# Kernel tuning notes

Measured on AMD Instinct MI355X. Metric: run time of the kernel, lower is better.

Reference implementation:

```python
import jax, jax.numpy as jnp
import numpy as np

ACTIVE_TASK = 0
K = 4  # top-k experts

def setup_inputs() -> dict:
    key = jax.random.key(0)
    k1, k2, k3, k4 = jax.random.split(key, 4)
    B, L, H, E, T = 16, 8192, 768, 16, 8
    x = jax.random.normal(k1, (B, L, H), jnp.float32)
    task_full = jax.random.normal(k2, (T, H), jnp.float32)
    gate_w = jax.random.normal(k3, (H, E), jnp.float32) * 0.02   # f_gate Linear weight (transposed)
    gate_b = jnp.zeros((E,), jnp.float32)                         # f_gate Linear bias
    expert_w = jax.random.normal(k4, (E, H, H), jnp.float32) * 0.02  # ParallelExperts weight [E, in, out]
    return {"x": x, "task_full": task_full, "gate_w": gate_w, "gate_b": gate_b, "expert_w": expert_w}

def reference(x, task_full, gate_w, gate_b, expert_w):
    T = task_full.shape[0]
    E = gate_w.shape[1]
    # f_gate = SiLU -> Linear
    logits = jax.nn.silu(task_full) @ gate_w + gate_b            # [T, E]
    probs = jax.nn.softmax(logits, axis=1)                       # [T, E]
    top_k_gates, top_k_indices = jax.lax.top_k(probs, K)         # [T, K]
    # probs_full_quantized: one-hot mask of selected experts per task
    probs_full_quantized = jnp.zeros((T, E), jnp.float32).at[
        jnp.arange(T)[:, None], top_k_indices].set(1.0)
    active_probs = probs[ACTIVE_TASK]                            # [E]
    gates = top_k_gates[ACTIVE_TASK]                             # [K]
    idx = top_k_indices[ACTIVE_TASK]                             # [K] int
    # compute_gating on a single task row: batch_index = arange(K)//K == 0 for all
    # slots, so every selected expert consumes a copy of x[0] (length rows each),
    # and index_add accumulates all K weighted expert outputs into out[0].
    h = jnp.einsum('ld,kdo->klo', x[0], expert_w[idx])           # grouped expert GEMM [K, L, H]
    out0 = jnp.einsum('k,klo->lo', gates, h)                     # gate-weighted combine [L, H]
    out = jnp.zeros_like(x).at[0].add(out0)                      # scatter-add at batch_index (all 0)
    return 1.0 + out, active_probs, probs_full_quantized
```

## Files before the change

### kernel.cpp

```cpp
#include <hip/hip_runtime.h>
#include <hip/hip_bf16.h>

typedef __attribute__((ext_vector_type(8))) short short8;
typedef __attribute__((ext_vector_type(4))) float f32x4;

#define H_DIM 768
#define E_EXP 16
#define T_TASK 8
#define KSEL 4
#define L_SEQ 8192
#define B_BATCH 16
#define EW_STRIDE (768*768)

#define WCT_BLOCKS 576
#define FILLA_BLOCKS 1472
#define GEMM_BLOCKS 384
#define FILLB_BLOCKS 1472
#define AS_LD 40

__device__ __forceinline__ void gating_block(
    const float* __restrict__ task_full,
    const float* __restrict__ gate_w,
    const float* __restrict__ gate_b,
    float* silu_s, float (*logits)[E_EXP],
    float* g_sh, int* i_sh,
    float* __restrict__ out_tail, bool write_tail) {
  const int tid = threadIdx.x;
  for (int i = tid; i < T_TASK * H_DIM; i += 256) {
    float v = task_full[i];
    silu_s[i] = v / (1.f + expf(-v));
  }
  __syncthreads();
  if (tid < T_TASK * E_EXP) {
    const int t = tid >> 4, e = tid & 15;
    float a0 = 0.f, a1 = 0.f, a2 = 0.f, a3 = 0.f;
    const float* sl = &silu_s[t * H_DIM];
    for (int h = 0; h < H_DIM; h += 4) {
      a0 += sl[h]     * gate_w[(h)     * E_EXP + e];
      a1 += sl[h + 1] * gate_w[(h + 1) * E_EXP + e];
      a2 += sl[h + 2] * gate_w[(h + 2) * E_EXP + e];
      a3 += sl[h + 3] * gate_w[(h + 3) * E_EXP + e];
    }
    logits[t][e] = (a0 + a1) + (a2 + a3) + gate_b[e];
  }
  __syncthreads();
  if (tid < T_TASK) {
    const int t = tid;
    float p[E_EXP];
    float m = -1e30f;
    for (int e = 0; e < E_EXP; ++e) m = fmaxf(m, logits[t][e]);
    float s = 0.f;
    for (int e = 0; e < E_EXP; ++e) { p[e] = expf(logits[t][e] - m); s += p[e]; }
    const float inv = 1.f / s;
    for (int e = 0; e < E_EXP; ++e) p[e] *= inv;
    bool used[E_EXP];
    for (int e = 0; e < E_EXP; ++e) used[e] = false;
    float g[KSEL]; int sel[KSEL];
    for (int k = 0; k < KSEL; ++k) {
      float bv = -1.f; int bi = 0;
      for (int e = 0; e < E_EXP; ++e)
        if (!used[e] && p[e] > bv) { bv = p[e]; bi = e; }
      used[bi] = true; sel[k] = bi; g[k] = bv;
    }
    if (write_tail) {
      for (int e = 0; e < E_EXP; ++e)
        out_tail[E_EXP + t * E_EXP + e] = used[e] ? 1.f : 0.f;
      if (t == 0)
        for (int e = 0; e < E_EXP; ++e) out_tail[e] = p[e];
    }
    if (t == 0)
      for (int k = 0; k < KSEL; ++k) { g_sh[k] = g[k]; i_sh[k] = sel[k]; }
  }
  __syncthreads();
}

__global__ __launch_bounds__(256) void kA_wct_fill(
    const float* __restrict__ task_full,
    const float* __restrict__ gate_w,
    const float* __restrict__ gate_b,
    const float* __restrict__ expert_w,
    __hip_bfloat16* __restrict__ wct,
    float* __restrict__ out_tail,
    float4* __restrict__ fill_p, size_t fill_n4) {
  const int bid = blockIdx.x;
  const int tid = threadIdx.x;
  if (bid < WCT_BLOCKS) {
    __shared__ float silu_s[T_TASK * H_DIM];
    __shared__ float logits[T_TASK][E_EXP];
    __shared__ float g_sh[KSEL];
    __shared__ int   i_sh[KSEL];
    __shared__ float tile[32][33];
    gating_block(task_full, gate_w, gate_b, silu_s, logits, g_sh, i_sh,
                 out_tail, bid == 0);
    const float g0 = g_sh[0], g1 = g_sh[1], g2 = g_sh[2], g3 = g_sh[3];
    const size_t e0 = (size_t)i_sh[0] * EW_STRIDE;
    const size_t e1 = (size_t)i_sh[1] * EW_STRIDE;
    const size_t e2 = (size_t)i_sh[2] * EW_STRIDE;
    const size_t e3 = (size_t)i_sh[3] * EW_STRIDE;
    const int d0 = (bid % 24) * 32, o0 = (bid / 24) * 32;
    const int c = tid & 31;
    const int r0 = tid >> 5;
#pragma unroll
    for (int it = 0; it < 4; ++it) {
      const int rr = it * 8 + r0;
      const size_t off = (size_t)(d0 + rr) * H_DIM + o0 + c;
      tile[rr][c] = g0 * expert_w[e0 + off] + g1 * expert_w[e1 + off] +
                    g2 * expert_w[e2 + off] + g3 * expert_w[e3 + off];
    }
    __syncthreads();
#pragma unroll
    for (int it = 0; it < 4; ++it) {
      const int rr = it * 8 + r0;
      wct[(size_t)(o0 + rr) * H_DIM + d0 + c] = __float2bfloat16(tile[c][rr]);
    }
  } else {
    const int fb = bid - WCT_BLOCKS;
    size_t i = (size_t)fb * 256 + tid;
    const size_t stride = (size_t)FILLA_BLOCKS * 256;
    const float4 one = make_float4(1.f, 1.f, 1.f, 1.f);
    for (; i < fill_n4; i += stride) fill_p[i] = one;
  }
}

__device__ __forceinline__ void gload_lds16(const void* g, void* l) {
  __builtin_amdgcn_global_load_lds((const __attribute__((address_space(1))) void*)g,
                                   (__attribute__((address_space(3))) void*)l, 16, 0, 0);
}

__global__ __launch_bounds__(256) void kB_gemm_fill(
    const float* __restrict__ X,
    const __hip_bfloat16* __restrict__ Bt,
    float* __restrict__ C,
    float4* __restrict__ fill_p, size_t fill_n4) {
  const int bid = blockIdx.x;
  const int tid = threadIdx.x;
  if (bid < GEMM_BLOCKS) {
    __shared__ __hip_bfloat16 As[128 * AS_LD];
    __shared__ __hip_bfloat16 Bs[128 * 32];
    const int m0 = (bid & 63) * 128;
    const int n0 = (bid >> 6) * 128;
    const int lane = tid & 63;
    const int w = tid >> 6;
    const int wr = w >> 1, wc = w & 1;
    const int ra = tid >> 1, sa = tid & 1;
    const int rb = tid >> 2, sb = tid & 3;
    const float* gx = X + (size_t)(m0 + ra) * H_DIM + sa * 16;
    const __hip_bfloat16* gb = Bt + (size_t)(n0 + rb) * H_DIM + sb * 8;
    f32x4 acc[4][4] = {};
    const int arow = wr * 64 + (lane & 15);
    const int brow = wc * 64 + (lane & 15);
    const int koff = (lane >> 4) * 8;
    for (int k0 = 0; k0 < H_DIM; k0 += 32) {
      gload_lds16(gb + k0,              &Bs[tid * 8]);
      gload_lds16(gb + 64 * H_DIM + k0, &Bs[2048 + tid * 8]);
      const float4 f0 = *(const float4*)(gx + k0);
      const float4 f1 = *(const float4*)(gx + k0 + 4);
      const float4 f2 = *(const float4*)(gx + k0 + 8);
      const float4 f3 = *(const float4*)(gx + k0 + 12);
      alignas(16) __hip_bfloat16 hb[16];
      hb[0]  = __float2bfloat16(f0.x); hb[1]  = __float2bfloat16(f0.y);
      hb[2]  = __float2bfloat16(f0.z); hb[3]  = __float2bfloat16(f0.w);
      hb[4]  = __float2bfloat16(f1.x); hb[5]  = __float2bfloat16(f1.y);
      hb[6]  = __float2bfloat16(f1.z); hb[7]  = __float2bfloat16(f1.w);
      hb[8]  = __float2bfloat16(f2.x); hb[9]  = __float2bfloat16(f2.y);
      hb[10] = __float2bfloat16(f2.z); hb[11] = __float2bfloat16(f2.w);
      hb[12] = __float2bfloat16(f3.x); hb[13] = __float2bfloat16(f3.y);
      hb[14] = __float2bfloat16(f3.z); hb[15] = __float2bfloat16(f3.w);
      *(uint4*)&As[ra * AS_LD + sa * 16]     = *(const uint4*)&hb[0];
      *(uint4*)&As[ra * AS_LD + sa * 16 + 8] = *(const uint4*)&hb[8];
      __syncthreads();
      short8 av[4], bv[4];
#pragma unroll
      for (int i = 0; i < 4; ++i) av[i] = *(const short8*)&As[(arow + i * 16) * AS_LD + koff];
#pragma unroll
      for (int j = 0; j < 4; ++j) bv[j] = *(const short8*)&Bs[(brow + j * 16) * 32 + koff];
#pragma unroll
      for (int i = 0; i < 4; ++i)
#pragma unroll
        for (int j = 0; j < 4; ++j)
          acc[i][j] = __builtin_amdgcn_mfma_f32_16x16x32_bf16(av[i], bv[j], acc[i][j], 0, 0, 0);
      __syncthreads();
    }
    const int crow0 = m0 + wr * 64 + (lane >> 4) * 4;
    const int ccol0 = n0 + wc * 64 + (lane & 15);
#pragma unroll
    for (int i = 0; i < 4; ++i)
#pragma unroll
      for (int j = 0; j < 4; ++j)
#pragma unroll
        for (int q = 0; q < 4; ++q)
          C[(size_t)(crow0 + i * 16 + q) * H_DIM + ccol0 + j * 16] = 1.0f + acc[i][j][q];
  } else {
    const int fb = bid - GEMM_BLOCKS;
    size_t i = (size_t)fb * 256 + tid;
    const size_t stride = (size_t)FILLB_BLOCKS * 256;
    const float4 one = make_float4(1.f, 1.f, 1.f, 1.f);
    for (; i < fill_n4; i += stride) fill_p[i] = one;
  }
}

extern "C" void kernel_launch(void* const* d_in, const int* in_sizes, int n_in,
                              void* d_out, int out_size, void* d_ws, size_t ws_size,
                              hipStream_t stream) {
  const float* x         = (const float*)d_in[0];
  const float* task_full = (const float*)d_in[1];
  const float* gate_w    = (const float*)d_in[2];
  const float* gate_b    = (const float*)d_in[3];
  const float* expert_w  = (const float*)d_in[4];
  float* out = (float*)d_out;

  const size_t n_out_main = (size_t)B_BATCH * L_SEQ * H_DIM;
  float* out_tail = out + n_out_main;

  __hip_bfloat16* wct = (__hip_bfloat16*)d_ws;

  const size_t fillA_n4 = (size_t)8 * L_SEQ * H_DIM / 4;
  kA_wct_fill<<<WCT_BLOCKS + FILLA_BLOCKS, 256, 0, stream>>>(
      task_full, gate_w, gate_b, expert_w, wct, out_tail,
      (float4*)(out + (size_t)1 * L_SEQ * H_DIM), fillA_n4);

  const size_t fillB_n4 = (size_t)7 * L_SEQ * H_DIM / 4;
  kB_gemm_fill<<<GEMM_BLOCKS + FILLB_BLOCKS, 256, 0, stream>>>(
      x, wct, out,
      (float4*)(out + (size_t)9 * L_SEQ * H_DIM), fillB_n4);
}
```

Measured before the change: 128.5 us.

## Fuse weight-combine, GEMM and fill into one kernel with atomic flag handoff

Merges the two launches into a single persistent-style kernel: weight-combine blocks publish completion through an agent-scope atomic counter, GEMM blocks spin on it, and fill blocks write ones concurrently. It also unions the shared-memory layouts and switches the output and fill stores to nontemporal. The goal is to remove the kernel boundary and let the big fill overlap the whole pipeline. In exchange it adds a memset launch and a spin-wait, and it can deadlock if GEMM blocks occupy the machine before the producer blocks are scheduled.

```diff
diff --git a/kernel.cpp b/kernel.cpp
--- a/kernel.cpp
+++ b/kernel.cpp
@@ -13,90 +13,97 @@
 #define EW_STRIDE (768*768)
 
 #define WCT_BLOCKS 576
-#define FILLA_BLOCKS 1472
 #define GEMM_BLOCKS 384
-#define FILLB_BLOCKS 1472
+#define FILL_BLOCKS 1536
+#define TOTAL_BLOCKS (WCT_BLOCKS + GEMM_BLOCKS + FILL_BLOCKS)
 #define AS_LD 40
-
-__device__ __forceinline__ void gating_block(
-    const float* __restrict__ task_full,
-    const float* __restrict__ gate_w,
-    const float* __restrict__ gate_b,
-    float* silu_s, float (*logits)[E_EXP],
-    float* g_sh, int* i_sh,
-    float* __restrict__ out_tail, bool write_tail) {
-  const int tid = threadIdx.x;
-  for (int i = tid; i < T_TASK * H_DIM; i += 256) {
-    float v = task_full[i];
-    silu_s[i] = v / (1.f + expf(-v));
-  }
-  __syncthreads();
-  if (tid < T_TASK * E_EXP) {
-    const int t = tid >> 4, e = tid & 15;
-    float a0 = 0.f, a1 = 0.f, a2 = 0.f, a3 = 0.f;
-    const float* sl = &silu_s[t * H_DIM];
-    for (int h = 0; h < H_DIM; h += 4) {
-      a0 += sl[h]     * gate_w[(h)     * E_EXP + e];
-      a1 += sl[h + 1] * gate_w[(h + 1) * E_EXP + e];
-      a2 += sl[h + 2] * gate_w[(h + 2) * E_EXP + e];
-      a3 += sl[h + 3] * gate_w[(h + 3) * E_EXP + e];
-    }
-    logits[t][e] = (a0 + a1) + (a2 + a3) + gate_b[e];
-  }
-  __syncthreads();
-  if (tid < T_TASK) {
-    const int t = tid;
-    float p[E_EXP];
-    float m = -1e30f;
-    for (int e = 0; e < E_EXP; ++e) m = fmaxf(m, logits[t][e]);
-    float s = 0.f;
-    for (int e = 0; e < E_EXP; ++e) { p[e] = expf(logits[t][e] - m); s += p[e]; }
-    const float inv = 1.f / s;
-    for (int e = 0; e < E_EXP; ++e) p[e] *= inv;
-    bool used[E_EXP];
-    for (int e = 0; e < E_EXP; ++e) used[e] = false;
-    float g[KSEL]; int sel[KSEL];
-    for (int k = 0; k < KSEL; ++k) {
-      float bv = -1.f; int bi = 0;
-      for (int e = 0; e < E_EXP; ++e)
-        if (!used[e] && p[e] > bv) { bv = p[e]; bi = e; }
-      used[bi] = true; sel[k] = bi; g[k] = bv;
-    }
-    if (write_tail) {
-      for (int e = 0; e < E_EXP; ++e)
-        out_tail[E_EXP + t * E_EXP + e] = used[e] ? 1.f : 0.f;
-      if (t == 0)
-        for (int e = 0; e < E_EXP; ++e) out_tail[e] = p[e];
-    }
-    if (t == 0)
-      for (int k = 0; k < KSEL; ++k) { g_sh[k] = g[k]; i_sh[k] = sel[k]; }
-  }
-  __syncthreads();
+#define FLAG_OFF 1572864
+
+union SMemU {
+  struct {
+    unsigned short As[128 * AS_LD];
+    unsigned short Bs[128 * 32];
+  } g;
+  struct {
+    float silu[T_TASK * H_DIM];
+    float logits[T_TASK][E_EXP];
+    float tile[32][33];
+    float g_sh[KSEL];
+    int   i_sh[KSEL];
+  } w;
+};
+
+__device__ __forceinline__ void gload_lds16(const void* g, void* l) {
+  __builtin_amdgcn_global_load_lds((const __attribute__((address_space(1))) void*)g,
+                                   (__attribute__((address_space(3))) void*)l, 16, 0, 0);
 }
 
-__global__ __launch_bounds__(256) void kA_wct_fill(
+__global__ __launch_bounds__(256) void mega_kernel(
+    const float* __restrict__ x,
     const float* __restrict__ task_full,
     const float* __restrict__ gate_w,
     const float* __restrict__ gate_b,
     const float* __restrict__ expert_w,
     __hip_bfloat16* __restrict__ wct,
-    float* __restrict__ out_tail,
-    float4* __restrict__ fill_p, size_t fill_n4) {
+    int* __restrict__ flag,
+    float* __restrict__ out,
+    float* __restrict__ out_tail) {
+  __shared__ SMemU sm;
   const int bid = blockIdx.x;
   const int tid = threadIdx.x;
+
   if (bid < WCT_BLOCKS) {
-    __shared__ float silu_s[T_TASK * H_DIM];
-    __shared__ float logits[T_TASK][E_EXP];
-    __shared__ float g_sh[KSEL];
-    __shared__ int   i_sh[KSEL];
-    __shared__ float tile[32][33];
-    gating_block(task_full, gate_w, gate_b, silu_s, logits, g_sh, i_sh,
-                 out_tail, bid == 0);
-    const float g0 = g_sh[0], g1 = g_sh[1], g2 = g_sh[2], g3 = g_sh[3];
-    const size_t e0 = (size_t)i_sh[0] * EW_STRIDE;
-    const size_t e1 = (size_t)i_sh[1] * EW_STRIDE;
-    const size_t e2 = (size_t)i_sh[2] * EW_STRIDE;
-    const size_t e3 = (size_t)i_sh[3] * EW_STRIDE;
+    for (int i = tid; i < T_TASK * H_DIM; i += 256) {
+      float v = task_full[i];
+      sm.w.silu[i] = v / (1.f + expf(-v));
+    }
+    __syncthreads();
+    if (tid < T_TASK * E_EXP) {
+      const int t = tid >> 4, e = tid & 15;
+      float a0 = 0.f, a1 = 0.f, a2 = 0.f, a3 = 0.f;
+      const float* sl = &sm.w.silu[t * H_DIM];
+      for (int h = 0; h < H_DIM; h += 4) {
+        a0 += sl[h]     * gate_w[(h)     * E_EXP + e];
+        a1 += sl[h + 1] * gate_w[(h + 1) * E_EXP + e];
+        a2 += sl[h + 2] * gate_w[(h + 2) * E_EXP + e];
+        a3 += sl[h + 3] * gate_w[(h + 3) * E_EXP + e];
+      }
+      sm.w.logits[t][e] = (a0 + a1) + (a2 + a3) + gate_b[e];
+    }
+    __syncthreads();
+    if (tid < T_TASK) {
+      const int t = tid;
+      float p[E_EXP];
+      float m = -1e30f;
+      for (int e = 0; e < E_EXP; ++e) m = fmaxf(m, sm.w.logits[t][e]);
+      float s = 0.f;
+      for (int e = 0; e < E_EXP; ++e) { p[e] = expf(sm.w.logits[t][e] - m); s += p[e]; }
+      const float inv = 1.f / s;
+      for (int e = 0; e < E_EXP; ++e) p[e] *= inv;
+      bool used[E_EXP];
+      for (int e = 0; e < E_EXP; ++e) used[e] = false;
+      float g[KSEL]; int sel[KSEL];
+      for (int k = 0; k < KSEL; ++k) {
+        float bv = -1.f; int bi = 0;
+        for (int e = 0; e < E_EXP; ++e)
+          if (!used[e] && p[e] > bv) { bv = p[e]; bi = e; }
+        used[bi] = true; sel[k] = bi; g[k] = bv;
+      }
+      if (bid == 0) {
+        for (int e = 0; e < E_EXP; ++e)
+          out_tail[E_EXP + t * E_EXP + e] = used[e] ? 1.f : 0.f;
+        if (t == 0)
+          for (int e = 0; e < E_EXP; ++e) out_tail[e] = p[e];
+      }
+      if (t == 0)
+        for (int k = 0; k < KSEL; ++k) { sm.w.g_sh[k] = g[k]; sm.w.i_sh[k] = sel[k]; }
+    }
+    __syncthreads();
+    const float g0 = sm.w.g_sh[0], g1 = sm.w.g_sh[1], g2 = sm.w.g_sh[2], g3 = sm.w.g_sh[3];
+    const size_t e0 = (size_t)sm.w.i_sh[0] * EW_STRIDE;
+    const size_t e1 = (size_t)sm.w.i_sh[1] * EW_STRIDE;
+    const size_t e2 = (size_t)sm.w.i_sh[2] * EW_STRIDE;
+    const size_t e3 = (size_t)sm.w.i_sh[3] * EW_STRIDE;
     const int d0 = (bid % 24) * 32, o0 = (bid / 24) * 32;
     const int c = tid & 31;
     const int r0 = tid >> 5;
@@ -104,55 +111,45 @@
     for (int it = 0; it < 4; ++it) {
       const int rr = it * 8 + r0;
       const size_t off = (size_t)(d0 + rr) * H_DIM + o0 + c;
-      tile[rr][c] = g0 * expert_w[e0 + off] + g1 * expert_w[e1 + off] +
-                    g2 * expert_w[e2 + off] + g3 * expert_w[e3 + off];
+      sm.w.tile[rr][c] = g0 * expert_w[e0 + off] + g1 * expert_w[e1 + off] +
+                         g2 * expert_w[e2 + off] + g3 * expert_w[e3 + off];
     }
     __syncthreads();
 #pragma unroll
     for (int it = 0; it < 4; ++it) {
       const int rr = it * 8 + r0;
-      wct[(size_t)(o0 + rr) * H_DIM + d0 + c] = __float2bfloat16(tile[c][rr]);
-    }
-  } else {
-    const int fb = bid - WCT_BLOCKS;
-    size_t i = (size_t)fb * 256 + tid;
-    const size_t stride = (size_t)FILLA_BLOCKS * 256;
-    const float4 one = make_float4(1.f, 1.f, 1.f, 1.f);
-    for (; i < fill_n4; i += stride) fill_p[i] = one;
-  }
-}
-
-__device__ __forceinline__ void gload_lds16(const void* g, void* l) {
-  __builtin_amdgcn_global_load_lds((const __attribute__((address_space(1))) void*)g,
-                                   (__attribute__((address_space(3))) void*)l, 16, 0, 0);
-}
-
-__global__ __launch_bounds__(256) void kB_gemm_fill(
-    const float* __restrict__ X,
-    const __hip_bfloat16* __restrict__ Bt,
-    float* __restrict__ C,
-    float4* __restrict__ fill_p, size_t fill_n4) {
-  const int bid = blockIdx.x;
-  const int tid = threadIdx.x;
-  if (bid < GEMM_BLOCKS) {
-    __shared__ __hip_bfloat16 As[128 * AS_LD];
-    __shared__ __hip_bfloat16 Bs[128 * 32];
-    const int m0 = (bid & 63) * 128;
-    const int n0 = (bid >> 6) * 128;
+      wct[(size_t)(o0 + rr) * H_DIM + d0 + c] = __float2bfloat16(sm.w.tile[c][rr]);
+    }
+    __threadfence();
+    __syncthreads();
+    if (tid == 0)
+      __hip_atomic_fetch_add(flag, 1, __ATOMIC_RELEASE, __HIP_MEMORY_SCOPE_AGENT);
+
+  } else if (bid < WCT_BLOCKS + GEMM_BLOCKS) {
+    if (tid == 0) {
+      while (__hip_atomic_load(flag, __ATOMIC_ACQUIRE, __HIP_MEMORY_SCOPE_AGENT) < WCT_BLOCKS)
+        __builtin_amdgcn_s_sleep(4);
+    }
+    __syncthreads();
+    __hip_bfloat16* As = (__hip_bfloat16*)sm.g.As;
+    __hip_bfloat16* Bs = (__hip_bfloat16*)sm.g.Bs;
+    const int gb = bid - WCT_BLOCKS;
+    const int m0 = (gb & 63) * 128;
+    const int n0 = (gb >> 6) * 128;
     const int lane = tid & 63;
     const int w = tid >> 6;
     const int wr = w >> 1, wc = w & 1;
     const int ra = tid >> 1, sa = tid & 1;
     const int rb = tid >> 2, sb = tid & 3;
-    const float* gx = X + (size_t)(m0 + ra) * H_DIM + sa * 16;
-    const __hip_bfloat16* gb = Bt + (size_t)(n0 + rb) * H_DIM + sb * 8;
+    const float* gx = x + (size_t)(m0 + ra) * H_DIM + sa * 16;
+    const __hip_bfloat16* gb_ptr = wct + (size_t)(n0 + rb) * H_DIM + sb * 8;
     f32x4 acc[4][4] = {};
     const int arow = wr * 64 + (lane & 15);
     const int brow = wc * 64 + (lane & 15);
     const int koff = (lane >> 4) * 8;
     for (int k0 = 0; k0 < H_DIM; k0 += 32) {
-      gload_lds16(gb + k0,              &Bs[tid * 8]);
-      gload_lds16(gb + 64 * H_DIM + k0, &Bs[2048 + tid * 8]);
+      gload_lds16(gb_ptr + k0,              &Bs[tid * 8]);
+      gload_lds16(gb_ptr + 64 * H_DIM + k0, &Bs[2048 + tid * 8]);
       const float4 f0 = *(const float4*)(gx + k0);
       const float4 f1 = *(const float4*)(gx + k0 + 4);
       const float4 f2 = *(const float4*)(gx + k0 + 8);
@@ -189,13 +186,18 @@
       for (int j = 0; j < 4; ++j)
 #pragma unroll
         for (int q = 0; q < 4; ++q)
-          C[(size_t)(crow0 + i * 16 + q) * H_DIM + ccol0 + j * 16] = 1.0f + acc[i][j][q];
+          __builtin_nontemporal_store(
+              1.0f + acc[i][j][q],
+              &out[(size_t)(crow0 + i * 16 + q) * H_DIM + ccol0 + j * 16]);
+
   } else {
-    const int fb = bid - GEMM_BLOCKS;
+    const int fb = bid - (WCT_BLOCKS + GEMM_BLOCKS);
+    f32x4* p = (f32x4*)(out + (size_t)L_SEQ * H_DIM);
+    const size_t n4 = (size_t)(B_BATCH - 1) * L_SEQ * H_DIM / 4;
     size_t i = (size_t)fb * 256 + tid;
-    const size_t stride = (size_t)FILLB_BLOCKS * 256;
-    const float4 one = make_float4(1.f, 1.f, 1.f, 1.f);
-    for (; i < fill_n4; i += stride) fill_p[i] = one;
+    const size_t stride = (size_t)FILL_BLOCKS * 256;
+    const f32x4 one = {1.f, 1.f, 1.f, 1.f};
+    for (; i < n4; i += stride) __builtin_nontemporal_store(one, &p[i]);
   }
 }
 
@@ -213,14 +215,9 @@
   float* out_tail = out + n_out_main;
 
   __hip_bfloat16* wct = (__hip_bfloat16*)d_ws;
-
-  const size_t fillA_n4 = (size_t)8 * L_SEQ * H_DIM / 4;
-  kA_wct_fill<<<WCT_BLOCKS + FILLA_BLOCKS, 256, 0, stream>>>(
-      task_full, gate_w, gate_b, expert_w, wct, out_tail,
-      (float4*)(out + (size_t)1 * L_SEQ * H_DIM), fillA_n4);
-
-  const size_t fillB_n4 = (size_t)7 * L_SEQ * H_DIM / 4;
-  kB_gemm_fill<<<GEMM_BLOCKS + FILLB_BLOCKS, 256, 0, stream>>>(
-      x, wct, out,
-      (float4*)(out + (size_t)9 * L_SEQ * H_DIM), fillB_n4);
+  int* flag = (int*)((char*)d_ws + FLAG_OFF);
+
+  hipMemsetAsync((void*)flag, 0, sizeof(int), stream);
+  mega_kernel<<<TOTAL_BLOCKS, 256, 0, stream>>>(
+      x, task_full, gate_w, gate_b, expert_w, wct, flag, out, out_tail);
 }
```

Measured after the change: 255.9 us. +99.2%, slower.
